# Kernel tuning notes

Hardware: AMD Instinct MI355X
Metric: run time of the kernel (lower is better)

The kernel has to match this reference:

```python
import jax, jax.numpy as jnp
import numpy as np

N_NODES = 100000
N_EDGES = 3200000
IN_F, HID, OUT_F = 512, 64, 64
K_HOPS = 10


def setup_inputs() -> dict:
    key = jax.random.key(0)
    k1, k2, k3, k4, k5 = jax.random.split(key, 5)
    x = jax.random.normal(k1, (N_NODES, IN_F), dtype=jnp.float32)
    edge_index = jax.random.randint(k2, (2, N_EDGES), 0, N_NODES, dtype=jnp.int64)
    # Glorot-ish scaled params (bias=False per init_kwargs)
    W1 = jax.random.normal(k3, (IN_F, HID), dtype=jnp.float32) / np.sqrt(IN_F)
    W2 = jax.random.normal(k4, (HID, OUT_F), dtype=jnp.float32) / np.sqrt(HID)
    s = jax.random.normal(k5, (OUT_F, 1), dtype=jnp.float32) / np.sqrt(OUT_F)
    return {"x": x, "edge_index": edge_index, "W1": W1, "W2": W2, "s": s}


def reference(x, edge_index, W1, W2, s):
    # --- MLP (dropout omitted: eval mode), relu applied after each linear per source ---
    h = jnp.maximum(x @ W1, 0.0)          # [N, HID]
    h = jnp.maximum(h @ W2, 0.0)          # [N, OUT_F]

    src = edge_index[0]
    dst = edge_index[1]
    n = h.shape[0]
    ones = jnp.ones(src.shape[0], dtype=h.dtype)
    deg_out = jax.ops.segment_sum(ones, src, num_segments=n)
    deg_in = jax.ops.segment_sum(ones, dst, num_segments=n)
    dinv_out = jnp.where(deg_out > 0, jax.lax.rsqrt(jnp.maximum(deg_out, 1.0)), 0.0)
    dinv_in = jnp.where(deg_in > 0, jax.lax.rsqrt(jnp.maximum(deg_in, 1.0)), 0.0)
    norm = dinv_out[src] * dinv_in[dst]   # [E] symmetric normalization

    # --- K-hop propagation: D^{-1/2} A D^{-1/2} applied K times ---
    hops = [h]
    feat = h
    for _ in range(K_HOPS):  # small fixed K, unrolled
        msg = feat[src] * norm[:, None]                          # gather [E, F]
        feat = jax.ops.segment_sum(msg, dst, num_segments=n)     # scatter [N, F]
        hops.append(feat)
    H = jnp.stack(hops, axis=1)            # [N, K+1, F]

    # --- adaptive hop combination via sigmoid gate ---
    scores = jax.nn.sigmoid(H @ s)         # [N, K+1, 1]
    out = jnp.sum(scores * H, axis=1)      # [N, F]
    return out
```

## Files before the change

### kernel.cpp

```cpp
#include <hip/hip_runtime.h>
#include <hip/hip_bf16.h>

#define N_NODES 100000
#define N_EDGES 3200000
#define IN_F 512
#define HID 64
#define OUT_F 64
#define K_HOPS 10
#define N_SCAN_BLOCKS ((N_NODES + 255) / 256)

#define HIST_BLOCKS 64
#define HIST_BINS 32768
#define HIST_WORDS (HIST_BINS / 2)
#define EDGES_PER_HIST_BLOCK (N_EDGES / HIST_BLOCKS)

#define NBKT 224
#define NBN  448
#define BKT_CAP 16384
#define BKZ_BLOCKS 256
#define EDGES_PER_BKZ_BLOCK (N_EDGES / BKZ_BLOCKS)
#define BKZ_BATCH 8192

typedef __attribute__((ext_vector_type(8))) short bf16x8;
typedef __attribute__((ext_vector_type(4))) float f32x4;

static __device__ __forceinline__ unsigned short f2bf(float f) {
    unsigned int u = __float_as_uint(f);
    u += 0x7FFFu + ((u >> 16) & 1u);
    return (unsigned short)(u >> 16);
}
static __device__ __forceinline__ float bf2f(unsigned short s) {
    return __uint_as_float(((unsigned int)s) << 16);
}

__global__ void detect_i32_kernel(const unsigned int* ei_words, int* flag_is32) {
    int i = blockIdx.x * blockDim.x + threadIdx.x;
    unsigned int w = ei_words[2 * i + 1];
    if (w != 0u) atomicOr(flag_is32, 1);
}

__global__ void __launch_bounds__(256) convert_kernel(const void* ei_raw, const int* flag_is32,
                                                      int* __restrict__ src32,
                                                      int* __restrict__ dst32) {
    int t = blockIdx.x * blockDim.x + threadIdx.x;
    if (t >= N_EDGES / 2) return;
    if (*flag_is32) {
        const int2* ei = (const int2*)ei_raw;
        *(int2*)(src32 + 2 * t) = ei[t];
        *(int2*)(dst32 + 2 * t) = ei[N_EDGES / 2 + t];
    } else {
        const longlong2* ei = (const longlong2*)ei_raw;
        longlong2 s = ei[t];
        longlong2 d = ei[N_EDGES / 2 + t];
        *(int2*)(src32 + 2 * t) = make_int2((int)s.x, (int)s.y);
        *(int2*)(dst32 + 2 * t) = make_int2((int)d.x, (int)d.y);
    }
}

__global__ void __launch_bounds__(256) hist_kernel(const int* __restrict__ src32,
                                                   const int* __restrict__ dst32,
                                                   unsigned int* __restrict__ partials) {
    __shared__ unsigned int cnt[HIST_WORDS];
    int tid = threadIdx.x;
    for (int w = tid; w < HIST_WORDS; w += 256) cnt[w] = 0u;
    __syncthreads();

    int arr = blockIdx.y >> 2;
    int range = blockIdx.y & 3;
    unsigned lo = (unsigned)(range * HIST_BINS);
    const int* a = arr ? dst32 : src32;
    int beg = blockIdx.x * EDGES_PER_HIST_BLOCK;
    int end = beg + EDGES_PER_HIST_BLOCK;
    for (int i = beg + tid; i < end; i += 256) {
        unsigned v = (unsigned)a[i] - lo;
        if (v < HIST_BINS) atomicAdd(&cnt[v >> 1], 1u << ((v & 1u) * 16u));
    }
    __syncthreads();

    unsigned int* outp = partials + ((size_t)(blockIdx.y * HIST_BLOCKS + blockIdx.x)) * HIST_WORDS;
    for (int w = tid; w < HIST_WORDS / 4; w += 256)
        ((uint4*)outp)[w] = ((const uint4*)cnt)[w];
}

__global__ void __launch_bounds__(256) hist_scan_kernel(const unsigned int* __restrict__ partials,
                                                        float* __restrict__ dinv,
                                                        int* __restrict__ deg,
                                                        int arr) {
    int wg = blockIdx.x * blockDim.x + threadIdx.x;
    if (wg >= 4 * HIST_WORDS) return;
    int range = wg >> 14;
    int word = wg & (HIST_WORDS - 1);
    const unsigned int* base = partials + ((size_t)(arr * 4 + range) * HIST_BLOCKS) * HIST_WORDS + word;
    unsigned lo = 0, hi = 0;
    for (int b = 0; b < HIST_BLOCKS; ++b) {
        unsigned c = base[(size_t)b * HIST_WORDS];
        lo += c & 0xffffu;
        hi += c >> 16;
    }
    int v0 = range * HIST_BINS + 2 * word;
    if (v0 < N_NODES) {
        dinv[v0] = lo ? rsqrtf((float)lo) : 0.0f;
        if (deg) deg[v0] = (int)lo;
    }
    int v1 = v0 + 1;
    if (v1 < N_NODES) {
        dinv[v1] = hi ? rsqrtf((float)hi) : 0.0f;
        if (deg) deg[v1] = (int)hi;
    }
}

__global__ void block_sum_kernel(const int* __restrict__ deg, int* __restrict__ partial) {
    __shared__ int s[256];
    int t = threadIdx.x;
    int i = blockIdx.x * 256 + t;
    s[t] = (i < N_NODES) ? deg[i] : 0;
    __syncthreads();
    for (int off = 128; off >= 1; off >>= 1) {
        if (t < off) s[t] += s[t + off];
        __syncthreads();
    }
    if (t == 0) partial[blockIdx.x] = s[0];
}

__global__ void scan_partial_kernel(int* partial, int* row_start) {
    if (threadIdx.x == 0 && blockIdx.x == 0) {
        int acc = 0;
        for (int b = 0; b < N_SCAN_BLOCKS; ++b) {
            int v = partial[b];
            partial[b] = acc;
            acc += v;
        }
        row_start[N_NODES] = acc;
    }
}

__global__ void row_start_kernel(const int* __restrict__ deg, const int* __restrict__ partial,
                                 int* __restrict__ row_start) {
    __shared__ int s[256];
    int t = threadIdx.x;
    int i = blockIdx.x * 256 + t;
    int v = (i < N_NODES) ? deg[i] : 0;
    s[t] = v;
    __syncthreads();
    for (int off = 1; off < 256; off <<= 1) {
        int add = (t >= off) ? s[t - off] : 0;
        __syncthreads();
        s[t] += add;
        __syncthreads();
    }
    if (i < N_NODES) row_start[i] = s[t] - v + partial[blockIdx.x];
}

__global__ void bucket_init_kernel(const int* __restrict__ row_start,
                                   int* __restrict__ bucket_start,
                                   int* __restrict__ gcur) {
    int t = blockIdx.x * blockDim.x + threadIdx.x;
    if (t <= NBKT) {
        int node = t * NBN;
        if (node > N_NODES) node = N_NODES;
        int v = row_start[node];
        bucket_start[t] = v;
        if (t < NBKT) gcur[t] = v;
    }
}

__global__ void __launch_bounds__(256) bucketize_kernel(const int* __restrict__ src32,
                                                        const int* __restrict__ dst32,
                                                        int* __restrict__ gcur,
                                                        int* __restrict__ entries) {
    __shared__ unsigned int stag[BKZ_BATCH];
    __shared__ unsigned char stagb[BKZ_BATCH];
    __shared__ int cnt[256], sAr[256], ofs_l[256], gbase_l[256];

    int tid = threadIdx.x;
    int beg = blockIdx.x * EDGES_PER_BKZ_BLOCK;

    for (int bb = 0; bb < EDGES_PER_BKZ_BLOCK; bb += BKZ_BATCH) {
        int bn = min(BKZ_BATCH, EDGES_PER_BKZ_BLOCK - bb);
        cnt[tid] = 0;
        __syncthreads();

        unsigned pk[32];
#pragma unroll
        for (int j = 0; j < 32; ++j) {
            int loc = j * 256 + tid;
            pk[j] = 0xFFFFFFFFu;
            if (loc < bn) {
                int d = dst32[beg + bb + loc];
                int b = d / NBN;
                int dl = d - b * NBN;
                int off = atomicAdd(&cnt[b], 1);
                pk[j] = ((unsigned)b << 22) | ((unsigned)dl << 13) | (unsigned)off;
            }
        }
        __syncthreads();
        int c = cnt[tid];
        sAr[tid] = c;
        __syncthreads();
        for (int off = 1; off < 256; off <<= 1) {
            int add = (tid >= off) ? sAr[tid - off] : 0;
            __syncthreads();
            sAr[tid] += add;
            __syncthreads();
        }
        ofs_l[tid] = sAr[tid] - c;
        if (tid < NBKT && c > 0) gbase_l[tid] = atomicAdd(&gcur[tid], c);
        __syncthreads();

#pragma unroll
        for (int j = 0; j < 32; ++j) {
            int loc = j * 256 + tid;
            if (loc < bn && pk[j] != 0xFFFFFFFFu) {
                int s = src32[beg + bb + loc];
                int b = pk[j] >> 22;
                int dl = (pk[j] >> 13) & 511;
                int off = pk[j] & 8191;
                int pos = ofs_l[b] + off;
                stag[pos] = ((unsigned)s << 9) | (unsigned)dl;
                stagb[pos] = (unsigned char)b;
            }
        }
        __syncthreads();
        for (int i = tid; i < bn; i += 256) {
            int b = stagb[i];
            entries[gbase_l[b] + (i - ofs_l[b])] = (int)stag[i];
        }
        __syncthreads();
    }
}

__global__ void __launch_bounds__(1024) sort_kernel(const int* __restrict__ entries,
                                                    const int* __restrict__ bucket_start,
                                                    const int* __restrict__ row_start,
                                                    int* __restrict__ srcs) {
    extern __shared__ int sbuf[];
    int* sin = sbuf;
    int* sout = sbuf + BKT_CAP;
    int* cur = sbuf + 2 * BKT_CAP;
    int tid = threadIdx.x;
    int b = blockIdx.x;
    int ebeg = bucket_start[b];
    int eend = bucket_start[b + 1];
    int n = eend - ebeg;

    for (int i = tid; i < n; i += 1024) sin[i] = entries[ebeg + i];
    for (int r = tid; r < NBN; r += 1024) {
        int node = b * NBN + r;
        cur[r] = ((node < N_NODES) ? row_start[node] : eend) - ebeg;
    }
    __syncthreads();
    for (int i = tid; i < n; i += 1024) {
        int e = sin[i];
        int pos = atomicAdd(&cur[e & 511], 1);
        sout[pos] = (int)((unsigned)e >> 9);
    }
    __syncthreads();
    for (int i = tid; i < n; i += 1024) srcs[ebeg + i] = sout[i];
}

__global__ void __launch_bounds__(256) mlp_kernel(const float* __restrict__ x,
                                                  const float* __restrict__ W1,
                                                  const float* __restrict__ W2,
                                                  const float* __restrict__ sv,
                                                  const float* __restrict__ dinv_out,
                                                  float* __restrict__ out,
                                                  unsigned short* __restrict__ g0) {
    __shared__ __align__(16) unsigned short b1[8 * 4 * 64 * 8];
    __shared__ __align__(16) unsigned short b2[2 * 4 * 64 * 8];
    __shared__ __align__(16) unsigned short a2s[4][2 * 64 * 8];

    int tid = threadIdx.x;
    int w = tid >> 6;
    int l = tid & 63;
    int kg = l >> 4;
    int m  = l & 15;
    int row0 = blockIdx.x * 64;
    int row = row0 + w * 16 + m;
    bool valid = row < N_NODES;
    const float* xp = x + (size_t)row * IN_F + kg * 8;

#pragma unroll
    for (int i = 0; i < 4; ++i) {
        int flat = i * 1024 + tid * 4;
        float4 v = *(const float4*)(W2 + flat);
        int r = flat >> 6, c0 = flat & 63;
        int t2 = r >> 5, kgs = (r >> 3) & 3, ko = r & 7;
        float vv[4] = {v.x, v.y, v.z, v.w};
#pragma unroll
        for (int q = 0; q < 4; ++q) {
            int cc = c0 + q;
            b2[(((t2 * 4 + (cc >> 4)) * 64) + (kgs * 16 + (cc & 15))) * 8 + ko] = f2bf(vv[q]);
        }
    }

    f32x4 acc[4];
#pragma unroll
    for (int nt = 0; nt < 4; ++nt) acc[nt] = (f32x4){0.f, 0.f, 0.f, 0.f};

    for (int p = 0; p < 2; ++p) {
        __syncthreads();
#pragma unroll
        for (int i = 0; i < 16; ++i) {
            int flat = i * 1024 + tid * 4;
            int rl = flat >> 6;
            int c0 = flat & 63;
            float4 v = *(const float4*)(W1 + (size_t)(p * 256 + rl) * HID + c0);
            int t = rl >> 5, kgs = (rl >> 3) & 3, ko = rl & 7;
            float vv[4] = {v.x, v.y, v.z, v.w};
#pragma unroll
            for (int q = 0; q < 4; ++q) {
                int cc = c0 + q;
                b1[(((t * 4 + (cc >> 4)) * 64) + (kgs * 16 + (cc & 15))) * 8 + ko] = f2bf(vv[q]);
            }
        }
        __syncthreads();
#pragma unroll
        for (int t = 0; t < 8; ++t) {
            union { bf16x8 v; unsigned short u[8]; } a;
            if (valid) {
                const float* ap = xp + (p * 256 + t * 32);
                float4 u0 = *(const float4*)ap;
                float4 u1 = *(const float4*)(ap + 4);
                a.u[0] = f2bf(u0.x); a.u[1] = f2bf(u0.y);
                a.u[2] = f2bf(u0.z); a.u[3] = f2bf(u0.w);
                a.u[4] = f2bf(u1.x); a.u[5] = f2bf(u1.y);
                a.u[6] = f2bf(u1.z); a.u[7] = f2bf(u1.w);
            } else {
#pragma unroll
                for (int q = 0; q < 8; ++q) a.u[q] = 0;
            }
#pragma unroll
            for (int nt = 0; nt < 4; ++nt) {
                bf16x8 b = *(const bf16x8*)&b1[((t * 4 + nt) * 64 + l) * 8];
                acc[nt] = __builtin_amdgcn_mfma_f32_16x16x32_bf16(a.v, b, acc[nt], 0, 0, 0);
            }
        }
    }

#pragma unroll
    for (int nt = 0; nt < 4; ++nt) {
#pragma unroll
        for (int reg = 0; reg < 4; ++reg) {
            float v = fmaxf(acc[nt][reg], 0.0f);
            int cc = nt * 16 + m;
            int r = kg * 4 + reg;
            a2s[w][((cc >> 5) * 64 + (((cc >> 3) & 3) * 16 + r)) * 8 + (cc & 7)] = f2bf(v);
        }
    }

    f32x4 acc2[4];
#pragma unroll
    for (int nt = 0; nt < 4; ++nt) acc2[nt] = (f32x4){0.f, 0.f, 0.f, 0.f};
#pragma unroll
    for (int t2 = 0; t2 < 2; ++t2) {
        bf16x8 a = *(const bf16x8*)&a2s[w][(t2 * 64 + l) * 8];
#pragma unroll
        for (int nt = 0; nt < 4; ++nt) {
            bf16x8 b = *(const bf16x8*)&b2[((t2 * 4 + nt) * 64 + l) * 8];
            acc2[nt] = __builtin_amdgcn_mfma_f32_16x16x32_bf16(a, b, acc2[nt], 0, 0, 0);
        }
    }

    float vals[4][4];
    float pr[4] = {0.f, 0.f, 0.f, 0.f};
#pragma unroll
    for (int nt = 0; nt < 4; ++nt) {
        float s_c = sv[nt * 16 + m];
#pragma unroll
        for (int reg = 0; reg < 4; ++reg) {
            float v = fmaxf(acc2[nt][reg], 0.0f);
            vals[nt][reg] = v;
            pr[reg] = fmaf(v, s_c, pr[reg]);
        }
    }
#pragma unroll
    for (int off = 1; off <= 8; off <<= 1) {
#pragma unroll
        for (int reg = 0; reg < 4; ++reg) pr[reg] += __shfl_xor(pr[reg], off, 64);
    }
#pragma unroll
    for (int reg = 0; reg < 4; ++reg) {
        int node = row0 + w * 16 + kg * 4 + reg;
        if (node < N_NODES) {
            float score = 1.0f / (1.0f + expf(-pr[reg]));
            float dv = dinv_out[node];
#pragma unroll
            for (int nt = 0; nt < 4; ++nt) {
                out[(size_t)node * OUT_F + nt * 16 + m] = score * vals[nt][reg];
                g0[(size_t)node * OUT_F + nt * 16 + m] = f2bf(dv * vals[nt][reg]);
            }
        }
    }
}

__global__ void __launch_bounds__(256) hop_kernel(
        const unsigned short* __restrict__ g_prev,
        const int* __restrict__ row_start,
        const int* __restrict__ srcs,
        const float* __restrict__ dinv_in,
        const float* __restrict__ dinv_out,
        const float* __restrict__ sv,
        unsigned short* __restrict__ g_next,
        float* __restrict__ out) {
    int lane = threadIdx.x & 63;
    int node = blockIdx.x * 4 + (threadIdx.x >> 6);
    if (node >= N_NODES) return;
    int beg = row_start[node];
    int end = row_start[node + 1];
    int slot = lane >> 3;
    int sub  = lane & 7;

    float acc[8];
#pragma unroll
    for (int j = 0; j < 8; ++j) acc[j] = 0.0f;

    for (int chunk = beg; chunk < end; chunk += 64) {
        int nrem = end - chunk;
        int es = (chunk + lane < end) ? srcs[chunk + lane] : 0;

        uint4 v[8];
#pragma unroll
        for (int g = 0; g < 8; ++g) {
            int s = __shfl(es, g * 8 + slot, 64);
            if (g * 8 + slot < nrem)
                v[g] = *(const uint4*)(g_prev + (size_t)s * OUT_F + sub * 8);
        }
#pragma unroll
        for (int g = 0; g < 8; ++g) {
            if (g * 8 + slot < nrem) {
                acc[0] += __uint_as_float(v[g].x << 16);
                acc[1] += __uint_as_float(v[g].x & 0xffff0000u);
                acc[2] += __uint_as_float(v[g].y << 16);
                acc[3] += __uint_as_float(v[g].y & 0xffff0000u);
                acc[4] += __uint_as_float(v[g].z << 16);
                acc[5] += __uint_as_float(v[g].z & 0xffff0000u);
                acc[6] += __uint_as_float(v[g].w << 16);
                acc[7] += __uint_as_float(v[g].w & 0xffff0000u);
            }
        }
    }
#pragma unroll
    for (int off = 8; off <= 32; off <<= 1) {
#pragma unroll
        for (int j = 0; j < 8; ++j) acc[j] += __shfl_xor(acc[j], off, 64);
    }
    float di = dinv_in[node];
    float dq = dinv_out[node];
    float fn[8];
#pragma unroll
    for (int j = 0; j < 8; ++j) fn[j] = di * acc[j];

    float4 s0 = *(const float4*)(sv + sub * 8);
    float4 s1 = *(const float4*)(sv + sub * 8 + 4);
    float p = fn[0] * s0.x + fn[1] * s0.y + fn[2] * s0.z + fn[3] * s0.w
            + fn[4] * s1.x + fn[5] * s1.y + fn[6] * s1.z + fn[7] * s1.w;
#pragma unroll
    for (int off = 1; off <= 4; off <<= 1) p += __shfl_xor(p, off, 64);
    float score = 1.0f / (1.0f + expf(-p));

    if (slot == 0) {
        uint4 wv;
        wv.x = (unsigned)f2bf(dq * fn[0]) | ((unsigned)f2bf(dq * fn[1]) << 16);
        wv.y = (unsigned)f2bf(dq * fn[2]) | ((unsigned)f2bf(dq * fn[3]) << 16);
        wv.z = (unsigned)f2bf(dq * fn[4]) | ((unsigned)f2bf(dq * fn[5]) << 16);
        wv.w = (unsigned)f2bf(dq * fn[6]) | ((unsigned)f2bf(dq * fn[7]) << 16);
        *(uint4*)(g_next + (size_t)node * OUT_F + sub * 8) = wv;
    } else if (slot == 1) {
        float4* op = (float4*)(out + (size_t)node * OUT_F + sub * 8);
        float4 o0 = op[0], o1 = op[1];
        o0.x = fmaf(score, fn[0], o0.x);
        o0.y = fmaf(score, fn[1], o0.y);
        o0.z = fmaf(score, fn[2], o0.z);
        o0.w = fmaf(score, fn[3], o0.w);
        o1.x = fmaf(score, fn[4], o1.x);
        o1.y = fmaf(score, fn[5], o1.y);
        o1.z = fmaf(score, fn[6], o1.z);
        o1.w = fmaf(score, fn[7], o1.w);
        op[0] = o0;
        op[1] = o1;
    }
}

extern "C" void kernel_launch(void* const* d_in, const int* in_sizes, int n_in,
                              void* d_out, int out_size, void* d_ws, size_t ws_size,
                              hipStream_t stream) {
    const float* x  = (const float*)d_in[0];
    const void*  ei = d_in[1];
    const float* W1 = (const float*)d_in[2];
    const float* W2 = (const float*)d_in[3];
    const float* sv = (const float*)d_in[4];
    float* out = (float*)d_out;

    char* p = (char*)d_ws;
    auto alloc = [&](size_t bytes) -> char* {
        char* r = p;
        p += (bytes + 255) & ~(size_t)255;
        return r;
    };
    unsigned short* gA = (unsigned short*)alloc(sizeof(unsigned short) * N_NODES * OUT_F);
    unsigned short* gB = (unsigned short*)alloc(sizeof(unsigned short) * N_NODES * OUT_F);
    int*   src32     = (int*)alloc(sizeof(int) * N_EDGES);
    int*   dst32     = (int*)alloc(sizeof(int) * N_EDGES);
    char*  shared_region = alloc(sizeof(unsigned int) * 8 * HIST_BLOCKS * HIST_WORDS);
    unsigned int* partials = (unsigned int*)shared_region;
    int*   entries_raw = (int*)shared_region;
    int*   srcs      = (int*)alloc(sizeof(int) * N_EDGES);
    int*   deg_in    = (int*)alloc(sizeof(int) * N_NODES);
    float* dinv_out  = (float*)alloc(sizeof(float) * N_NODES);
    float* dinv_in   = (float*)alloc(sizeof(float) * N_NODES);
    int*   row_start = (int*)alloc(sizeof(int) * (N_NODES + 1));
    int*   bucket_start = (int*)alloc(sizeof(int) * (NBKT + 1));
    int*   gcur      = (int*)alloc(sizeof(int) * NBKT);
    int*   partial   = (int*)alloc(sizeof(int) * N_SCAN_BLOCKS);
    int*   flag      = (int*)alloc(256);

    hipMemsetAsync(flag, 0, sizeof(int), stream);

    detect_i32_kernel<<<4, 256, 0, stream>>>((const unsigned int*)ei, flag);
    convert_kernel<<<(N_EDGES / 2 + 255) / 256, 256, 0, stream>>>(ei, flag, src32, dst32);

    hist_kernel<<<dim3(HIST_BLOCKS, 8), 256, 0, stream>>>(src32, dst32, partials);
    hist_scan_kernel<<<(4 * HIST_WORDS + 255) / 256, 256, 0, stream>>>(partials, dinv_out,
                                                                       nullptr, 0);
    hist_scan_kernel<<<(4 * HIST_WORDS + 255) / 256, 256, 0, stream>>>(partials, dinv_in,
                                                                       deg_in, 1);
    block_sum_kernel<<<N_SCAN_BLOCKS, 256, 0, stream>>>(deg_in, partial);
    scan_partial_kernel<<<1, 64, 0, stream>>>(partial, row_start);
    row_start_kernel<<<N_SCAN_BLOCKS, 256, 0, stream>>>(deg_in, partial, row_start);
    bucket_init_kernel<<<1, 256, 0, stream>>>(row_start, bucket_start, gcur);
    bucketize_kernel<<<BKZ_BLOCKS, 256, 0, stream>>>(src32, dst32, gcur, entries_raw);

    int sort_lds = (2 * BKT_CAP + NBN) * (int)sizeof(int);
    hipFuncSetAttribute((const void*)sort_kernel,
                        hipFuncAttributeMaxDynamicSharedMemorySize, sort_lds);
    sort_kernel<<<NBKT, 1024, sort_lds, stream>>>(entries_raw, bucket_start, row_start, srcs);

    int mlp_blocks = (N_NODES + 63) / 64;
    mlp_kernel<<<mlp_blocks, 256, 0, stream>>>(x, W1, W2, sv, dinv_out, out, gA);

    int node_blocks = (N_NODES + 3) / 4;
    unsigned short* cur = gA;
    unsigned short* nxt = gB;
    for (int hop = 0; hop < K_HOPS; ++hop) {
        hop_kernel<<<node_blocks, 256, 0, stream>>>(cur, row_start, srcs,
                                                    dinv_in, dinv_out, sv, nxt, out);
        unsigned short* t = cur; cur = nxt; nxt = t;
    }
}
```

Measured before the change: 843.4 us.

## Partition edges by source quarter so hop gathers stay cache-resident

```diff
diff --git a/kernel.cpp b/kernel.cpp
--- a/kernel.cpp
+++ b/kernel.cpp
@@ -20,6 +20,9 @@
 #define BKZ_BLOCKS 256
 #define EDGES_PER_BKZ_BLOCK (N_EDGES / BKZ_BLOCKS)
 #define BKZ_BATCH 8192
+#define QSIZE 25000
+#define HOP_BLOCKS 2048
+#define HOP_WAVES (HOP_BLOCKS * 4)
 
 typedef __attribute__((ext_vector_type(8))) short bf16x8;
 typedef __attribute__((ext_vector_type(4))) float f32x4;
@@ -229,14 +232,16 @@
     }
 }
 
+#define SORT_LDS_BYTES ((2 * BKT_CAP + 1792 + 512) * 4)
 __global__ void __launch_bounds__(1024) sort_kernel(const int* __restrict__ entries,
                                                     const int* __restrict__ bucket_start,
-                                                    const int* __restrict__ row_start,
-                                                    int* __restrict__ srcs) {
+                                                    int* __restrict__ srcs,
+                                                    uint2* __restrict__ qoff) {
     extern __shared__ int sbuf[];
-    int* sin = sbuf;
+    int* sin  = sbuf;
     int* sout = sbuf + BKT_CAP;
-    int* cur = sbuf + 2 * BKT_CAP;
+    int* cnt  = sbuf + 2 * BKT_CAP;
+    int* nsum = cnt + 1792;
     int tid = threadIdx.x;
     int b = blockIdx.x;
     int ebeg = bucket_start[b];
@@ -244,15 +249,47 @@
     int n = eend - ebeg;
 
     for (int i = tid; i < n; i += 1024) sin[i] = entries[ebeg + i];
-    for (int r = tid; r < NBN; r += 1024) {
-        int node = b * NBN + r;
-        cur[r] = ((node < N_NODES) ? row_start[node] : eend) - ebeg;
-    }
+    for (int i = tid; i < 1792; i += 1024) cnt[i] = 0;
+    if (tid < 512) nsum[tid] = 0;
     __syncthreads();
     for (int i = tid; i < n; i += 1024) {
-        int e = sin[i];
-        int pos = atomicAdd(&cur[e & 511], 1);
-        sout[pos] = (int)((unsigned)e >> 9);
+        unsigned e = (unsigned)sin[i];
+        int q = (int)(e >> 9) / QSIZE;
+        atomicAdd(&cnt[(e & 511) * 4 + q], 1);
+    }
+    __syncthreads();
+    int s0 = 0, s1 = 0, s2 = 0, s3 = 0;
+    if (tid < NBN) {
+        s0 = cnt[tid * 4]; s1 = cnt[tid * 4 + 1];
+        s2 = cnt[tid * 4 + 2]; s3 = cnt[tid * 4 + 3];
+        nsum[tid] = s0 + s1 + s2 + s3;
+    }
+    __syncthreads();
+    for (int off = 1; off < 512; off <<= 1) {
+        int v = (tid < 512 && tid >= off) ? nsum[tid - off] : 0;
+        __syncthreads();
+        if (tid < 512) nsum[tid] += v;
+        __syncthreads();
+    }
+    if (tid < NBN) {
+        int deg = s0 + s1 + s2 + s3;
+        int base = nsum[tid] - deg;
+        cnt[tid * 4 + 0] = base;
+        cnt[tid * 4 + 1] = base + s0;
+        cnt[tid * 4 + 2] = base + s0 + s1;
+        cnt[tid * 4 + 3] = base + s0 + s1 + s2;
+        int node = b * NBN + tid;
+        if (node < N_NODES)
+            qoff[node] = make_uint2((unsigned)s0 | ((unsigned)(s0 + s1) << 16),
+                                    (unsigned)(s0 + s1 + s2) | ((unsigned)deg << 16));
+    }
+    __syncthreads();
+    for (int i = tid; i < n; i += 1024) {
+        unsigned e = (unsigned)sin[i];
+        int src = (int)(e >> 9);
+        int q = src / QSIZE;
+        int pos = atomicAdd(&cnt[(e & 511) * 4 + q], 1);
+        sout[pos] = src;
     }
     __syncthreads();
     for (int i = tid; i < n; i += 1024) srcs[ebeg + i] = sout[i];
@@ -397,87 +434,117 @@
         const unsigned short* __restrict__ g_prev,
         const int* __restrict__ row_start,
         const int* __restrict__ srcs,
+        const uint2* __restrict__ qoff,
         const float* __restrict__ dinv_in,
         const float* __restrict__ dinv_out,
         const float* __restrict__ sv,
+        float* __restrict__ accbuf,
         unsigned short* __restrict__ g_next,
         float* __restrict__ out) {
     int lane = threadIdx.x & 63;
-    int node = blockIdx.x * 4 + (threadIdx.x >> 6);
-    if (node >= N_NODES) return;
-    int beg = row_start[node];
-    int end = row_start[node + 1];
+    int wid = blockIdx.x * 4 + (threadIdx.x >> 6);
     int slot = lane >> 3;
     int sub  = lane & 7;
 
-    float acc[8];
-#pragma unroll
-    for (int j = 0; j < 8; ++j) acc[j] = 0.0f;
-
-    for (int chunk = beg; chunk < end; chunk += 64) {
-        int nrem = end - chunk;
-        int es = (chunk + lane < end) ? srcs[chunk + lane] : 0;
-
-        uint4 v[8];
-#pragma unroll
-        for (int g = 0; g < 8; ++g) {
-            int s = __shfl(es, g * 8 + slot, 64);
-            if (g * 8 + slot < nrem)
-                v[g] = *(const uint4*)(g_prev + (size_t)s * OUT_F + sub * 8);
-        }
-#pragma unroll
-        for (int g = 0; g < 8; ++g) {
-            if (g * 8 + slot < nrem) {
-                acc[0] += __uint_as_float(v[g].x << 16);
-                acc[1] += __uint_as_float(v[g].x & 0xffff0000u);
-                acc[2] += __uint_as_float(v[g].y << 16);
-                acc[3] += __uint_as_float(v[g].y & 0xffff0000u);
-                acc[4] += __uint_as_float(v[g].z << 16);
-                acc[5] += __uint_as_float(v[g].z & 0xffff0000u);
-                acc[6] += __uint_as_float(v[g].w << 16);
-                acc[7] += __uint_as_float(v[g].w & 0xffff0000u);
-            }
-        }
-    }
-#pragma unroll
-    for (int off = 8; off <= 32; off <<= 1) {
-#pragma unroll
-        for (int j = 0; j < 8; ++j) acc[j] += __shfl_xor(acc[j], off, 64);
-    }
-    float di = dinv_in[node];
-    float dq = dinv_out[node];
-    float fn[8];
-#pragma unroll
-    for (int j = 0; j < 8; ++j) fn[j] = di * acc[j];
-
-    float4 s0 = *(const float4*)(sv + sub * 8);
-    float4 s1 = *(const float4*)(sv + sub * 8 + 4);
-    float p = fn[0] * s0.x + fn[1] * s0.y + fn[2] * s0.z + fn[3] * s0.w
-            + fn[4] * s1.x + fn[5] * s1.y + fn[6] * s1.z + fn[7] * s1.w;
-#pragma unroll
-    for (int off = 1; off <= 4; off <<= 1) p += __shfl_xor(p, off, 64);
-    float score = 1.0f / (1.0f + expf(-p));
-
-    if (slot == 0) {
-        uint4 wv;
-        wv.x = (unsigned)f2bf(dq * fn[0]) | ((unsigned)f2bf(dq * fn[1]) << 16);
-        wv.y = (unsigned)f2bf(dq * fn[2]) | ((unsigned)f2bf(dq * fn[3]) << 16);
-        wv.z = (unsigned)f2bf(dq * fn[4]) | ((unsigned)f2bf(dq * fn[5]) << 16);
-        wv.w = (unsigned)f2bf(dq * fn[6]) | ((unsigned)f2bf(dq * fn[7]) << 16);
-        *(uint4*)(g_next + (size_t)node * OUT_F + sub * 8) = wv;
-    } else if (slot == 1) {
-        float4* op = (float4*)(out + (size_t)node * OUT_F + sub * 8);
-        float4 o0 = op[0], o1 = op[1];
-        o0.x = fmaf(score, fn[0], o0.x);
-        o0.y = fmaf(score, fn[1], o0.y);
-        o0.z = fmaf(score, fn[2], o0.z);
-        o0.w = fmaf(score, fn[3], o0.w);
-        o1.x = fmaf(score, fn[4], o1.x);
-        o1.y = fmaf(score, fn[5], o1.y);
-        o1.z = fmaf(score, fn[6], o1.z);
-        o1.w = fmaf(score, fn[7], o1.w);
-        op[0] = o0;
-        op[1] = o1;
+#pragma unroll
+    for (int q = 0; q < 4; ++q) {
+        for (int node = wid; node < N_NODES; node += HOP_WAVES) {
+            int beg = row_start[node];
+            uint2 qo = qoff[node];
+            int o1 = (int)(qo.x & 0xffffu), o2 = (int)(qo.x >> 16);
+            int o3 = (int)(qo.y & 0xffffu), dg = (int)(qo.y >> 16);
+            int lo = (q == 0) ? 0 : (q == 1) ? o1 : (q == 2) ? o2 : o3;
+            int hi = (q == 0) ? o1 : (q == 1) ? o2 : (q == 2) ? o3 : dg;
+            int qb = beg + lo, qe = beg + hi;
+
+            float acc[8];
+#pragma unroll
+            for (int j = 0; j < 8; ++j) acc[j] = 0.0f;
+
+            for (int chunk = qb; chunk < qe; chunk += 64) {
+                int nrem = qe - chunk;
+                int es = (chunk + lane < qe) ? srcs[chunk + lane] : 0;
+                uint4 v[8];
+#pragma unroll
+                for (int g = 0; g < 8; ++g) {
+                    int s = __shfl(es, g * 8 + slot, 64);
+                    if (g * 8 + slot < nrem)
+                        v[g] = *(const uint4*)(g_prev + (size_t)s * OUT_F + sub * 8);
+                }
+#pragma unroll
+                for (int g = 0; g < 8; ++g) {
+                    if (g * 8 + slot < nrem) {
+                        acc[0] += __uint_as_float(v[g].x << 16);
+                        acc[1] += __uint_as_float(v[g].x & 0xffff0000u);
+                        acc[2] += __uint_as_float(v[g].y << 16);
+                        acc[3] += __uint_as_float(v[g].y & 0xffff0000u);
+                        acc[4] += __uint_as_float(v[g].z << 16);
+                        acc[5] += __uint_as_float(v[g].z & 0xffff0000u);
+                        acc[6] += __uint_as_float(v[g].w << 16);
+                        acc[7] += __uint_as_float(v[g].w & 0xffff0000u);
+                    }
+                }
+            }
+#pragma unroll
+            for (int off = 8; off <= 32; off <<= 1) {
+#pragma unroll
+                for (int j = 0; j < 8; ++j) acc[j] += __shfl_xor(acc[j], off, 64);
+            }
+
+            if (slot == 0) {
+                float* ap = accbuf + (size_t)node * OUT_F + sub * 8;
+                if (q == 0) {
+                    float4 w0 = make_float4(acc[0], acc[1], acc[2], acc[3]);
+                    float4 w1 = make_float4(acc[4], acc[5], acc[6], acc[7]);
+                    ((float4*)ap)[0] = w0;
+                    ((float4*)ap)[1] = w1;
+                } else if (q < 3) {
+                    float4 r0 = ((const float4*)ap)[0];
+                    float4 r1 = ((const float4*)ap)[1];
+                    r0.x += acc[0]; r0.y += acc[1]; r0.z += acc[2]; r0.w += acc[3];
+                    r1.x += acc[4]; r1.y += acc[5]; r1.z += acc[6]; r1.w += acc[7];
+                    ((float4*)ap)[0] = r0;
+                    ((float4*)ap)[1] = r1;
+                } else {
+                    float4 r0 = ((const float4*)ap)[0];
+                    float4 r1 = ((const float4*)ap)[1];
+                    float tot[8] = {r0.x + acc[0], r0.y + acc[1], r0.z + acc[2], r0.w + acc[3],
+                                    r1.x + acc[4], r1.y + acc[5], r1.z + acc[6], r1.w + acc[7]};
+                    float di = dinv_in[node];
+                    float dq_ = dinv_out[node];
+                    float fn[8];
+#pragma unroll
+                    for (int j = 0; j < 8; ++j) fn[j] = di * tot[j];
+                    float4 s0 = *(const float4*)(sv + sub * 8);
+                    float4 s1 = *(const float4*)(sv + sub * 8 + 4);
+                    float p = fn[0] * s0.x + fn[1] * s0.y + fn[2] * s0.z + fn[3] * s0.w
+                            + fn[4] * s1.x + fn[5] * s1.y + fn[6] * s1.z + fn[7] * s1.w;
+#pragma unroll
+                    for (int off = 1; off <= 4; off <<= 1) p += __shfl_xor(p, off, 64);
+                    float score = 1.0f / (1.0f + expf(-p));
+
+                    float4* op = (float4*)(out + (size_t)node * OUT_F + sub * 8);
+                    float4 o0 = op[0], o1v = op[1];
+                    o0.x = fmaf(score, fn[0], o0.x);
+                    o0.y = fmaf(score, fn[1], o0.y);
+                    o0.z = fmaf(score, fn[2], o0.z);
+                    o0.w = fmaf(score, fn[3], o0.w);
+                    o1v.x = fmaf(score, fn[4], o1v.x);
+                    o1v.y = fmaf(score, fn[5], o1v.y);
+                    o1v.z = fmaf(score, fn[6], o1v.z);
+                    o1v.w = fmaf(score, fn[7], o1v.w);
+                    op[0] = o0;
+                    op[1] = o1v;
+
+                    uint4 wv;
+                    wv.x = (unsigned)f2bf(dq_ * fn[0]) | ((unsigned)f2bf(dq_ * fn[1]) << 16);
+                    wv.y = (unsigned)f2bf(dq_ * fn[2]) | ((unsigned)f2bf(dq_ * fn[3]) << 16);
+                    wv.z = (unsigned)f2bf(dq_ * fn[4]) | ((unsigned)f2bf(dq_ * fn[5]) << 16);
+                    wv.w = (unsigned)f2bf(dq_ * fn[6]) | ((unsigned)f2bf(dq_ * fn[7]) << 16);
+                    *(uint4*)(g_next + (size_t)node * OUT_F + sub * 8) = wv;
+                }
+            }
+        }
     }
 }
 
@@ -504,7 +571,9 @@
     char*  shared_region = alloc(sizeof(unsigned int) * 8 * HIST_BLOCKS * HIST_WORDS);
     unsigned int* partials = (unsigned int*)shared_region;
     int*   entries_raw = (int*)shared_region;
+    float* accbuf    = (float*)shared_region;
     int*   srcs      = (int*)alloc(sizeof(int) * N_EDGES);
+    uint2* qoff      = (uint2*)alloc(sizeof(uint2) * (size_t)NBKT * NBN);
     int*   deg_in    = (int*)alloc(sizeof(int) * N_NODES);
     float* dinv_out  = (float*)alloc(sizeof(float) * N_NODES);
     float* dinv_in   = (float*)alloc(sizeof(float) * N_NODES);
@@ -530,20 +599,19 @@
     bucket_init_kernel<<<1, 256, 0, stream>>>(row_start, bucket_start, gcur);
     bucketize_kernel<<<BKZ_BLOCKS, 256, 0, stream>>>(src32, dst32, gcur, entries_raw);
 
-    int sort_lds = (2 * BKT_CAP + NBN) * (int)sizeof(int);
     hipFuncSetAttribute((const void*)sort_kernel,
-                        hipFuncAttributeMaxDynamicSharedMemorySize, sort_lds);
-    sort_kernel<<<NBKT, 1024, sort_lds, stream>>>(entries_raw, bucket_start, row_start, srcs);
+                        hipFuncAttributeMaxDynamicSharedMemorySize, SORT_LDS_BYTES);
+    sort_kernel<<<NBKT, 1024, SORT_LDS_BYTES, stream>>>(entries_raw, bucket_start, srcs, qoff);
 
     int mlp_blocks = (N_NODES + 63) / 64;
     mlp_kernel<<<mlp_blocks, 256, 0, stream>>>(x, W1, W2, sv, dinv_out, out, gA);
 
-    int node_blocks = (N_NODES + 3) / 4;
     unsigned short* cur = gA;
     unsigned short* nxt = gB;
     for (int hop = 0; hop < K_HOPS; ++hop) {
-        hop_kernel<<<node_blocks, 256, 0, stream>>>(cur, row_start, srcs,
-                                                    dinv_in, dinv_out, sv, nxt, out);
+        hop_kernel<<<HOP_BLOCKS, 256, 0, stream>>>(cur, row_start, srcs, qoff,
+                                                   dinv_in, dinv_out, sv,
+                                                   accbuf, nxt, out);
         unsigned short* t = cur; cur = nxt; nxt = t;
     }
 }
```

New measurement: 2.291 ms. +171.6%, slower.

## Derive in-degrees and row offsets inside bucket sort instead of global histogram scan

Applied to the files above, without the earlier changes.

```diff
diff --git a/kernel.cpp b/kernel.cpp
--- a/kernel.cpp
+++ b/kernel.cpp
@@ -7,7 +7,6 @@
 #define HID 64
 #define OUT_F 64
 #define K_HOPS 10
-#define N_SCAN_BLOCKS ((N_NODES + 255) / 256)
 
 #define HIST_BLOCKS 64
 #define HIST_BINS 32768
@@ -57,18 +56,15 @@
     }
 }
 
-__global__ void __launch_bounds__(256) hist_kernel(const int* __restrict__ src32,
-                                                   const int* __restrict__ dst32,
+__global__ void __launch_bounds__(256) hist_kernel(const int* __restrict__ a,
                                                    unsigned int* __restrict__ partials) {
     __shared__ unsigned int cnt[HIST_WORDS];
     int tid = threadIdx.x;
     for (int w = tid; w < HIST_WORDS; w += 256) cnt[w] = 0u;
     __syncthreads();
 
-    int arr = blockIdx.y >> 2;
-    int range = blockIdx.y & 3;
+    int range = blockIdx.y;
     unsigned lo = (unsigned)(range * HIST_BINS);
-    const int* a = arr ? dst32 : src32;
     int beg = blockIdx.x * EDGES_PER_HIST_BLOCK;
     int end = beg + EDGES_PER_HIST_BLOCK;
     for (int i = beg + tid; i < end; i += 256) {
@@ -83,14 +79,12 @@
 }
 
 __global__ void __launch_bounds__(256) hist_scan_kernel(const unsigned int* __restrict__ partials,
-                                                        float* __restrict__ dinv,
-                                                        int* __restrict__ deg,
-                                                        int arr) {
+                                                        float* __restrict__ dinv) {
     int wg = blockIdx.x * blockDim.x + threadIdx.x;
     if (wg >= 4 * HIST_WORDS) return;
     int range = wg >> 14;
     int word = wg & (HIST_WORDS - 1);
-    const unsigned int* base = partials + ((size_t)(arr * 4 + range) * HIST_BLOCKS) * HIST_WORDS + word;
+    const unsigned int* base = partials + ((size_t)range * HIST_BLOCKS) * HIST_WORDS + word;
     unsigned lo = 0, hi = 0;
     for (int b = 0; b < HIST_BLOCKS; ++b) {
         unsigned c = base[(size_t)b * HIST_WORDS];
@@ -98,49 +92,34 @@
         hi += c >> 16;
     }
     int v0 = range * HIST_BINS + 2 * word;
-    if (v0 < N_NODES) {
-        dinv[v0] = lo ? rsqrtf((float)lo) : 0.0f;
-        if (deg) deg[v0] = (int)lo;
-    }
+    if (v0 < N_NODES) dinv[v0] = lo ? rsqrtf((float)lo) : 0.0f;
     int v1 = v0 + 1;
-    if (v1 < N_NODES) {
-        dinv[v1] = hi ? rsqrtf((float)hi) : 0.0f;
-        if (deg) deg[v1] = (int)hi;
-    }
-}
-
-__global__ void block_sum_kernel(const int* __restrict__ deg, int* __restrict__ partial) {
+    if (v1 < N_NODES) dinv[v1] = hi ? rsqrtf((float)hi) : 0.0f;
+}
+
+__global__ void __launch_bounds__(256) bucket_cnt_kernel(const int* __restrict__ dst32,
+                                                         int* __restrict__ bucket_cnt) {
+    __shared__ int c[NBKT];
+    int tid = threadIdx.x;
+    if (tid < NBKT) c[tid] = 0;
+    __syncthreads();
+    int beg = blockIdx.x * EDGES_PER_BKZ_BLOCK;
+    int end = beg + EDGES_PER_BKZ_BLOCK;
+    for (int i = beg + tid; i < end; i += 256) {
+        atomicAdd(&c[dst32[i] / NBN], 1);
+    }
+    __syncthreads();
+    if (tid < NBKT && c[tid] > 0) atomicAdd(&bucket_cnt[tid], c[tid]);
+}
+
+__global__ void __launch_bounds__(256) bucket_scan_kernel(const int* __restrict__ bucket_cnt,
+                                                          int* __restrict__ bucket_start,
+                                                          int* __restrict__ gcur,
+                                                          int* __restrict__ row_start) {
     __shared__ int s[256];
     int t = threadIdx.x;
-    int i = blockIdx.x * 256 + t;
-    s[t] = (i < N_NODES) ? deg[i] : 0;
-    __syncthreads();
-    for (int off = 128; off >= 1; off >>= 1) {
-        if (t < off) s[t] += s[t + off];
-        __syncthreads();
-    }
-    if (t == 0) partial[blockIdx.x] = s[0];
-}
-
-__global__ void scan_partial_kernel(int* partial, int* row_start) {
-    if (threadIdx.x == 0 && blockIdx.x == 0) {
-        int acc = 0;
-        for (int b = 0; b < N_SCAN_BLOCKS; ++b) {
-            int v = partial[b];
-            partial[b] = acc;
-            acc += v;
-        }
-        row_start[N_NODES] = acc;
-    }
-}
-
-__global__ void row_start_kernel(const int* __restrict__ deg, const int* __restrict__ partial,
-                                 int* __restrict__ row_start) {
-    __shared__ int s[256];
-    int t = threadIdx.x;
-    int i = blockIdx.x * 256 + t;
-    int v = (i < N_NODES) ? deg[i] : 0;
-    s[t] = v;
+    int c = (t < NBKT) ? bucket_cnt[t] : 0;
+    s[t] = c;
     __syncthreads();
     for (int off = 1; off < 256; off <<= 1) {
         int add = (t >= off) ? s[t - off] : 0;
@@ -148,19 +127,14 @@
         s[t] += add;
         __syncthreads();
     }
-    if (i < N_NODES) row_start[i] = s[t] - v + partial[blockIdx.x];
-}
-
-__global__ void bucket_init_kernel(const int* __restrict__ row_start,
-                                   int* __restrict__ bucket_start,
-                                   int* __restrict__ gcur) {
-    int t = blockIdx.x * blockDim.x + threadIdx.x;
-    if (t <= NBKT) {
-        int node = t * NBN;
-        if (node > N_NODES) node = N_NODES;
-        int v = row_start[node];
-        bucket_start[t] = v;
-        if (t < NBKT) gcur[t] = v;
+    if (t < NBKT) {
+        int excl = s[t] - c;
+        bucket_start[t] = excl;
+        gcur[t] = excl;
+        if (t == NBKT - 1) {
+            bucket_start[NBKT] = s[t];
+            row_start[N_NODES] = s[t];
+        }
     }
 }
 
@@ -229,14 +203,17 @@
     }
 }
 
+#define SORT_LDS_BYTES ((2 * BKT_CAP + 512 + 512) * 4)
 __global__ void __launch_bounds__(1024) sort_kernel(const int* __restrict__ entries,
                                                     const int* __restrict__ bucket_start,
-                                                    const int* __restrict__ row_start,
-                                                    int* __restrict__ srcs) {
+                                                    int* __restrict__ srcs,
+                                                    int* __restrict__ row_start,
+                                                    float* __restrict__ dinv_in) {
     extern __shared__ int sbuf[];
-    int* sin = sbuf;
+    int* sin  = sbuf;
     int* sout = sbuf + BKT_CAP;
-    int* cur = sbuf + 2 * BKT_CAP;
+    int* cnt  = sbuf + 2 * BKT_CAP;
+    int* nsum = cnt + 512;
     int tid = threadIdx.x;
     int b = blockIdx.x;
     int ebeg = bucket_start[b];
@@ -244,15 +221,35 @@
     int n = eend - ebeg;
 
     for (int i = tid; i < n; i += 1024) sin[i] = entries[ebeg + i];
-    for (int r = tid; r < NBN; r += 1024) {
-        int node = b * NBN + r;
-        cur[r] = ((node < N_NODES) ? row_start[node] : eend) - ebeg;
-    }
+    if (tid < 512) { cnt[tid] = 0; nsum[tid] = 0; }
     __syncthreads();
     for (int i = tid; i < n; i += 1024) {
-        int e = sin[i];
-        int pos = atomicAdd(&cur[e & 511], 1);
-        sout[pos] = (int)((unsigned)e >> 9);
+        atomicAdd(&cnt[(unsigned)sin[i] & 511u], 1);
+    }
+    __syncthreads();
+    int c = (tid < 512) ? cnt[tid] : 0;
+    if (tid < 512) nsum[tid] = c;
+    __syncthreads();
+    for (int off = 1; off < 512; off <<= 1) {
+        int v = (tid < 512 && tid >= off) ? nsum[tid - off] : 0;
+        __syncthreads();
+        if (tid < 512) nsum[tid] += v;
+        __syncthreads();
+    }
+    if (tid < NBN) {
+        int excl = nsum[tid] - c;
+        cnt[tid] = excl;
+        int node = b * NBN + tid;
+        if (node < N_NODES) {
+            row_start[node] = ebeg + excl;
+            dinv_in[node] = c ? rsqrtf((float)c) : 0.0f;
+        }
+    }
+    __syncthreads();
+    for (int i = tid; i < n; i += 1024) {
+        unsigned e = (unsigned)sin[i];
+        int pos = atomicAdd(&cnt[e & 511u], 1);
+        sout[pos] = (int)(e >> 9);
     }
     __syncthreads();
     for (int i = tid; i < n; i += 1024) srcs[ebeg + i] = sout[i];
@@ -501,39 +498,35 @@
     unsigned short* gB = (unsigned short*)alloc(sizeof(unsigned short) * N_NODES * OUT_F);
     int*   src32     = (int*)alloc(sizeof(int) * N_EDGES);
     int*   dst32     = (int*)alloc(sizeof(int) * N_EDGES);
-    char*  shared_region = alloc(sizeof(unsigned int) * 8 * HIST_BLOCKS * HIST_WORDS);
+    char*  shared_region = alloc(sizeof(unsigned int) * 4 * HIST_BLOCKS * HIST_WORDS);
     unsigned int* partials = (unsigned int*)shared_region;
     int*   entries_raw = (int*)shared_region;
     int*   srcs      = (int*)alloc(sizeof(int) * N_EDGES);
-    int*   deg_in    = (int*)alloc(sizeof(int) * N_NODES);
     float* dinv_out  = (float*)alloc(sizeof(float) * N_NODES);
     float* dinv_in   = (float*)alloc(sizeof(float) * N_NODES);
     int*   row_start = (int*)alloc(sizeof(int) * (N_NODES + 1));
+    int*   bucket_cnt   = (int*)alloc(sizeof(int) * NBKT);
     int*   bucket_start = (int*)alloc(sizeof(int) * (NBKT + 1));
     int*   gcur      = (int*)alloc(sizeof(int) * NBKT);
-    int*   partial   = (int*)alloc(sizeof(int) * N_SCAN_BLOCKS);
     int*   flag      = (int*)alloc(256);
 
     hipMemsetAsync(flag, 0, sizeof(int), stream);
+    hipMemsetAsync(bucket_cnt, 0, sizeof(int) * NBKT, stream);
 
     detect_i32_kernel<<<4, 256, 0, stream>>>((const unsigned int*)ei, flag);
     convert_kernel<<<(N_EDGES / 2 + 255) / 256, 256, 0, stream>>>(ei, flag, src32, dst32);
 
-    hist_kernel<<<dim3(HIST_BLOCKS, 8), 256, 0, stream>>>(src32, dst32, partials);
-    hist_scan_kernel<<<(4 * HIST_WORDS + 255) / 256, 256, 0, stream>>>(partials, dinv_out,
-                                                                       nullptr, 0);
-    hist_scan_kernel<<<(4 * HIST_WORDS + 255) / 256, 256, 0, stream>>>(partials, dinv_in,
-                                                                       deg_in, 1);
-    block_sum_kernel<<<N_SCAN_BLOCKS, 256, 0, stream>>>(deg_in, partial);
-    scan_partial_kernel<<<1, 64, 0, stream>>>(partial, row_start);
-    row_start_kernel<<<N_SCAN_BLOCKS, 256, 0, stream>>>(deg_in, partial, row_start);
-    bucket_init_kernel<<<1, 256, 0, stream>>>(row_start, bucket_start, gcur);
+    hist_kernel<<<dim3(HIST_BLOCKS, 4), 256, 0, stream>>>(src32, partials);
+    hist_scan_kernel<<<(4 * HIST_WORDS + 255) / 256, 256, 0, stream>>>(partials, dinv_out);
+
+    bucket_cnt_kernel<<<BKZ_BLOCKS, 256, 0, stream>>>(dst32, bucket_cnt);
+    bucket_scan_kernel<<<1, 256, 0, stream>>>(bucket_cnt, bucket_start, gcur, row_start);
     bucketize_kernel<<<BKZ_BLOCKS, 256, 0, stream>>>(src32, dst32, gcur, entries_raw);
 
-    int sort_lds = (2 * BKT_CAP + NBN) * (int)sizeof(int);
     hipFuncSetAttribute((const void*)sort_kernel,
-                        hipFuncAttributeMaxDynamicSharedMemorySize, sort_lds);
-    sort_kernel<<<NBKT, 1024, sort_lds, stream>>>(entries_raw, bucket_start, row_start, srcs);
+                        hipFuncAttributeMaxDynamicSharedMemorySize, SORT_LDS_BYTES);
+    sort_kernel<<<NBKT, 1024, SORT_LDS_BYTES, stream>>>(entries_raw, bucket_start,
+                                                        srcs, row_start, dinv_in);
 
     int mlp_blocks = (N_NODES + 63) / 64;
     mlp_kernel<<<mlp_blocks, 256, 0, stream>>>(x, W1, W2, sv, dinv_out, out, gA);
```

Measured after the change: 841.2 us. Within noise of the previous version (-0.3%).
